# Kernel tuning notes

Hardware: AMD Instinct MI355X
Metric: run time of the kernel (lower is better)

Reference implementation:

```python
import jax, jax.numpy as jnp
import numpy as np

NUM_HEADS = 8
H_NUM, W_NUM = 1, 2   # idx=0 stripe windows
SCALE = float((256 // NUM_HEADS) ** -0.5)  # qk_scale


def _partition(x, h_sp, w_sp):
    # x: (T,B,C,H,W) -> (T, B*nWin, heads, N, C//heads) with N = h_sp*w_sp
    T, B, C, H, W = x.shape
    x = x.reshape(T, B, C, H // h_sp, h_sp, W // w_sp, w_sp)
    x = x.transpose(0, 1, 3, 5, 4, 6, 2)  # T,B,nH,nW,h_sp,w_sp,C
    x = x.reshape(T, -1, h_sp * w_sp, NUM_HEADS, C // NUM_HEADS)
    return x.transpose(0, 1, 3, 2, 4)


def setup_inputs() -> dict:
    key = jax.random.key(0)
    k1, k2, k3 = jax.random.split(key, 3)
    shape = (4, 2, 256, 56, 56)
    return {
        "q": jax.random.normal(k1, shape, jnp.float32),
        "k": jax.random.normal(k2, shape, jnp.float32),
        "v": jax.random.normal(k3, shape, jnp.float32),
        "v_lamda": 1,
    }


def reference(q, k, v, v_lamda):
    T, B, C, H0, W0 = q.shape
    h_pad = (-H0) % H_NUM
    w_pad = (-W0) % W_NUM
    pad = ((0, 0), (0, 0), (0, 0), (0, h_pad), (0, w_pad))
    q = jnp.pad(q, pad)
    k = jnp.pad(k, pad)
    v = jnp.pad(v, pad)
    H, W = H0 + h_pad, W0 + w_pad
    h_sp, w_sp = H // H_NUM, W // W_NUM

    qw = _partition(q, h_sp, w_sp)  # (T, BnW, h, N, d)
    kw = _partition(k, h_sp, w_sp)
    vw = _partition(v, h_sp, w_sp)  # head dim = C*v_lamda//heads

    attn = jnp.einsum('twhnd,twhmd->twhnm', qw, kw)          # (QK^T), no softmax
    out = jnp.einsum('twhnm,twhmd->twhnd', attn, vw) * (SCALE * 2)

    # merge windows back: (T,BnW,h,N,d) -> (T,B,Cv,H,W)
    Cv = C * v_lamda
    out = out.transpose(0, 1, 3, 2, 4).reshape(T, -1, h_sp * w_sp, Cv)
    out = out.reshape(T, B, H_NUM, W_NUM, h_sp, w_sp, Cv)
    out = out.transpose(0, 1, 2, 4, 3, 5, 6).reshape(T, B, H, W, Cv)
    out = out.transpose(0, 1, 4, 2, 3)
    return out[:, :, :, :H0, :W0]
```

## Files before the change

### kernel.cpp

```cpp
#include <hip/hip_runtime.h>


#define TDIM 4
#define BDIM 2
#define CDIM 256
#define HDIM 56
#define WDIM 56
#define DHEAD 32
#define WSP 28
#define NPOS 1568
#define HW 3136
#define NPROB 128
#define SPLIT 4
#define NP_SPLIT 392
#define CHUNK 56
#define NCHUNK 7
#define LDSTRIDE 57
#define SCALE2 0.35355339059327373f

__global__ __launch_bounds__(256) void kv_kernel(const float* __restrict__ K,
                                                 const float* __restrict__ V,
                                                 float* __restrict__ M) {
    __shared__ float kT[32 * LDSTRIDE];
    __shared__ float vT[32 * LDSTRIDE];
    __shared__ float red[4 * 1024];

    const int blk  = blockIdx.x;
    const int p    = blk >> 2;
    const int s    = blk & 3;
    const int head = p & 7;
    const int win  = (p >> 3) & 1;
    const int b    = (p >> 4) & 1;
    const int t    = p >> 5;

    const long base = ((long)(t * BDIM + b) * CDIM + head * DHEAD) * HW;
    const float* __restrict__ Kb = K + base;
    const float* __restrict__ Vb = V + base;

    const int tid = threadIdx.x;
    const int l   = tid & 63;
    const int w   = tid >> 6;
    const int dd0 = (l >> 3) * 4;
    const int de0 = (l & 7) * 4;

    float acc[4][4] = {};

    const int n_base = s * NP_SPLIT;
    for (int c = 0; c < NCHUNK; ++c) {
        const int n0 = n_base + c * CHUNK;
        #pragma unroll
        for (int jj = 0; jj < 7; ++jj) {
            const int idx = tid + 256 * jj;
            const int ch  = idx / 56;
            const int pp  = idx - ch * 56;
            const int n   = n0 + pp;
            const int y   = n / 28;
            const int x   = win * 28 + (n - y * 28);
            const int ga  = ch * HW + y * WDIM + x;
            kT[ch * LDSTRIDE + pp] = Kb[ga];
            vT[ch * LDSTRIDE + pp] = Vb[ga];
        }
        __syncthreads();
        const int pbeg = w * 14;
        for (int pp = pbeg; pp < pbeg + 14; ++pp) {
            float kv[4], vv[4];
            #pragma unroll
            for (int i = 0; i < 4; ++i) kv[i] = kT[(dd0 + i) * LDSTRIDE + pp];
            #pragma unroll
            for (int j = 0; j < 4; ++j) vv[j] = vT[(de0 + j) * LDSTRIDE + pp];
            #pragma unroll
            for (int i = 0; i < 4; ++i)
                #pragma unroll
                for (int j = 0; j < 4; ++j)
                    acc[i][j] += kv[i] * vv[j];
        }
        __syncthreads();
    }

    #pragma unroll
    for (int i = 0; i < 4; ++i)
        #pragma unroll
        for (int j = 0; j < 4; ++j)
            red[w * 1024 + (dd0 + i) * 32 + (de0 + j)] = acc[i][j];
    __syncthreads();
    #pragma unroll
    for (int jj = 0; jj < 4; ++jj) {
        const int m = tid * 4 + jj;
        const float sum = red[m] + red[1024 + m] + red[2048 + m] + red[3072 + m];
        atomicAdd(&M[p * 1024 + m], sum);
    }
}

__global__ __launch_bounds__(256) void qm_kernel(const float* __restrict__ Q,
                                                 const float* __restrict__ M,
                                                 float* __restrict__ Out) {
    const int blk = blockIdx.x;
    const int p   = blk / 7;
    const int c   = blk - p * 7;
    const int n   = c * 256 + threadIdx.x;

    const int head = p & 7;
    const int win  = (p >> 3) & 1;
    const int b    = (p >> 4) & 1;
    const int t    = p >> 5;
    const float* __restrict__ Mp = M + p * 1024;

    if (n >= NPOS) return;

    const int y = n / 28;
    const int x = win * 28 + (n - y * 28);
    const long base = ((long)(t * BDIM + b) * CDIM + head * DHEAD) * HW
                    + y * WDIM + x;
    const float* __restrict__ Qb = Q + base;
    float* __restrict__ Ob = Out + base;

    float acc[32] = {};
    #pragma unroll 4
    for (int dd = 0; dd < 32; ++dd) {
        const float qv = Qb[dd * HW];
        #pragma unroll
        for (int de = 0; de < 32; ++de)
            acc[de] += qv * Mp[dd * 32 + de];
    }
    #pragma unroll
    for (int de = 0; de < 32; ++de)
        Ob[de * HW] = acc[de] * SCALE2;
}

extern "C" void kernel_launch(void* const* d_in, const int* in_sizes, int n_in,
                              void* d_out, int out_size, void* d_ws, size_t ws_size,
                              hipStream_t stream) {
    const float* q = (const float*)d_in[0];
    const float* k = (const float*)d_in[1];
    const float* v = (const float*)d_in[2];
    float* out = (float*)d_out;
    float* M   = (float*)d_ws;

    hipMemsetAsync(M, 0, NPROB * 1024 * sizeof(float), stream);
    kv_kernel<<<NPROB * SPLIT, 256, 0, stream>>>(k, v, M);
    qm_kernel<<<NPROB * 7, 256, 0, stream>>>(q, M, out);
}
```

Baseline: 132.9 us.

## Split KV reduction wider, write partials, reduce in QM kernel without atomics

The K^T V kernel now splits each problem into 14 blocks instead of 4. Each block loads its whole 112-position slice once into a transposed LDS layout so it can use float4 reads, and writes a per-block partial matrix instead of using atomicAdd. This removes the memset launch and the atomic contention. The QM kernel sums the 14 partials into shared memory, applies the scale there, and reads M with float4 loads from LDS. The trade-off is a larger workspace and repeated partial reduction in every QM block (7 blocks per problem), and 32 of the 256 threads in each QM block now idle.

```diff
diff --git a/kernel.cpp b/kernel.cpp
--- a/kernel.cpp
+++ b/kernel.cpp
@@ -1,130 +1,150 @@
 #include <hip/hip_runtime.h>
 
 
-#define TDIM 4
-#define BDIM 2
-#define CDIM 256
-#define HDIM 56
+#define HW 3136
 #define WDIM 56
-#define DHEAD 32
-#define WSP 28
 #define NPOS 1568
-#define HW 3136
 #define NPROB 128
-#define SPLIT 4
-#define NP_SPLIT 392
-#define CHUNK 56
-#define NCHUNK 7
-#define LDSTRIDE 57
+#define SPLIT 14
+#define PSPLIT 112
+#define LROW 36
 #define SCALE2 0.35355339059327373f
 
 __global__ __launch_bounds__(256) void kv_kernel(const float* __restrict__ K,
                                                  const float* __restrict__ V,
-                                                 float* __restrict__ M) {
-    __shared__ float kT[32 * LDSTRIDE];
-    __shared__ float vT[32 * LDSTRIDE];
-    __shared__ float red[4 * 1024];
+                                                 float* __restrict__ Mpart) {
+    __shared__ float lds[2 * PSPLIT * LROW];
+    float* kT = lds;
+    float* vT = lds + PSPLIT * LROW;
 
-    const int blk  = blockIdx.x;
-    const int p    = blk >> 2;
-    const int s    = blk & 3;
+    const int blk = blockIdx.x;
+    const int p   = blk / SPLIT;
+    const int s   = blk - p * SPLIT;
     const int head = p & 7;
     const int win  = (p >> 3) & 1;
     const int b    = (p >> 4) & 1;
     const int t    = p >> 5;
 
-    const long base = ((long)(t * BDIM + b) * CDIM + head * DHEAD) * HW;
+    const size_t base = (size_t)((t * 2 + b) * 256 + head * 32) * HW;
     const float* __restrict__ Kb = K + base;
     const float* __restrict__ Vb = V + base;
 
     const int tid = threadIdx.x;
+
+    #pragma unroll
+    for (int j = 0; j < 7; ++j) {
+        const int item = tid + 256 * j;
+        const int isv  = item >= 896 ? 1 : 0;
+        const int r    = item - isv * 896;
+        const int chg  = r / 112;
+        const int pp   = r - chg * 112;
+        const int n  = s * PSPLIT + pp;
+        const int y  = n / 28;
+        const int x  = n - y * 28;
+        const float* src = (isv ? Vb : Kb)
+                         + (size_t)chg * 4 * HW + y * WDIM + win * 28 + x;
+        float4 val;
+        val.x = src[0];
+        val.y = src[HW];
+        val.z = src[2 * HW];
+        val.w = src[3 * HW];
+        float* dst = isv ? vT : kT;
+        *(float4*)&dst[pp * LROW + chg * 4] = val;
+    }
+    __syncthreads();
+
     const int l   = tid & 63;
     const int w   = tid >> 6;
     const int dd0 = (l >> 3) * 4;
     const int de0 = (l & 7) * 4;
 
-    float acc[4][4] = {};
-
-    const int n_base = s * NP_SPLIT;
-    for (int c = 0; c < NCHUNK; ++c) {
-        const int n0 = n_base + c * CHUNK;
-        #pragma unroll
-        for (int jj = 0; jj < 7; ++jj) {
-            const int idx = tid + 256 * jj;
-            const int ch  = idx / 56;
-            const int pp  = idx - ch * 56;
-            const int n   = n0 + pp;
-            const int y   = n / 28;
-            const int x   = win * 28 + (n - y * 28);
-            const int ga  = ch * HW + y * WDIM + x;
-            kT[ch * LDSTRIDE + pp] = Kb[ga];
-            vT[ch * LDSTRIDE + pp] = Vb[ga];
-        }
-        __syncthreads();
-        const int pbeg = w * 14;
-        for (int pp = pbeg; pp < pbeg + 14; ++pp) {
-            float kv[4], vv[4];
-            #pragma unroll
-            for (int i = 0; i < 4; ++i) kv[i] = kT[(dd0 + i) * LDSTRIDE + pp];
-            #pragma unroll
-            for (int j = 0; j < 4; ++j) vv[j] = vT[(de0 + j) * LDSTRIDE + pp];
-            #pragma unroll
-            for (int i = 0; i < 4; ++i)
-                #pragma unroll
-                for (int j = 0; j < 4; ++j)
-                    acc[i][j] += kv[i] * vv[j];
-        }
-        __syncthreads();
+    float acc[4][4] = {{0.f}};
+    const int p0 = w * 28;
+    #pragma unroll 4
+    for (int pp = p0; pp < p0 + 28; ++pp) {
+        const float4 ka = *(const float4*)&kT[pp * LROW + dd0];
+        const float4 va = *(const float4*)&vT[pp * LROW + de0];
+        acc[0][0] += ka.x * va.x; acc[0][1] += ka.x * va.y;
+        acc[0][2] += ka.x * va.z; acc[0][3] += ka.x * va.w;
+        acc[1][0] += ka.y * va.x; acc[1][1] += ka.y * va.y;
+        acc[1][2] += ka.y * va.z; acc[1][3] += ka.y * va.w;
+        acc[2][0] += ka.z * va.x; acc[2][1] += ka.z * va.y;
+        acc[2][2] += ka.z * va.z; acc[2][3] += ka.z * va.w;
+        acc[3][0] += ka.w * va.x; acc[3][1] += ka.w * va.y;
+        acc[3][2] += ka.w * va.z; acc[3][3] += ka.w * va.w;
     }
+    __syncthreads();
 
     #pragma unroll
     for (int i = 0; i < 4; ++i)
         #pragma unroll
-        for (int j = 0; j < 4; ++j)
-            red[w * 1024 + (dd0 + i) * 32 + (de0 + j)] = acc[i][j];
+        for (int jj = 0; jj < 4; ++jj)
+            lds[w * 1024 + (dd0 + i) * 32 + (de0 + jj)] = acc[i][jj];
     __syncthreads();
-    #pragma unroll
-    for (int jj = 0; jj < 4; ++jj) {
-        const int m = tid * 4 + jj;
-        const float sum = red[m] + red[1024 + m] + red[2048 + m] + red[3072 + m];
-        atomicAdd(&M[p * 1024 + m], sum);
-    }
+
+    const float4 r0 = *(const float4*)&lds[tid * 4];
+    const float4 r1 = *(const float4*)&lds[1024 + tid * 4];
+    const float4 r2 = *(const float4*)&lds[2048 + tid * 4];
+    const float4 r3 = *(const float4*)&lds[3072 + tid * 4];
+    float4 o;
+    o.x = r0.x + r1.x + r2.x + r3.x;
+    o.y = r0.y + r1.y + r2.y + r3.y;
+    o.z = r0.z + r1.z + r2.z + r3.z;
+    o.w = r0.w + r1.w + r2.w + r3.w;
+    *(float4*)&Mpart[(size_t)blk * 1024 + tid * 4] = o;
 }
 
 __global__ __launch_bounds__(256) void qm_kernel(const float* __restrict__ Q,
-                                                 const float* __restrict__ M,
+                                                 const float* __restrict__ Mpart,
                                                  float* __restrict__ Out) {
+    __shared__ float M[1024];
     const int blk = blockIdx.x;
     const int p   = blk / 7;
     const int c   = blk - p * 7;
-    const int n   = c * 256 + threadIdx.x;
+    const int tid = threadIdx.x;
+
+    const float* mp = Mpart + (size_t)p * SPLIT * 1024 + tid * 4;
+    float4 sum = {0.f, 0.f, 0.f, 0.f};
+    #pragma unroll
+    for (int s = 0; s < SPLIT; ++s) {
+        const float4 v = *(const float4*)&mp[s * 1024];
+        sum.x += v.x; sum.y += v.y; sum.z += v.z; sum.w += v.w;
+    }
+    sum.x *= SCALE2; sum.y *= SCALE2; sum.z *= SCALE2; sum.w *= SCALE2;
+    *(float4*)&M[tid * 4] = sum;
+    __syncthreads();
 
     const int head = p & 7;
     const int win  = (p >> 3) & 1;
     const int b    = (p >> 4) & 1;
     const int t    = p >> 5;
-    const float* __restrict__ Mp = M + p * 1024;
 
-    if (n >= NPOS) return;
+    if (tid < 224) {
+        const int n = c * 224 + tid;
+        const int y = n / 28;
+        const int x = n - y * 28;
+        const size_t base = (size_t)((t * 2 + b) * 256 + head * 32) * HW
+                          + y * WDIM + win * 28 + x;
+        const float* __restrict__ Qb = Q + base;
+        float* __restrict__ Ob = Out + base;
 
-    const int y = n / 28;
-    const int x = win * 28 + (n - y * 28);
-    const long base = ((long)(t * BDIM + b) * CDIM + head * DHEAD) * HW
-                    + y * WDIM + x;
-    const float* __restrict__ Qb = Q + base;
-    float* __restrict__ Ob = Out + base;
-
-    float acc[32] = {};
-    #pragma unroll 4
-    for (int dd = 0; dd < 32; ++dd) {
-        const float qv = Qb[dd * HW];
+        float acc[32] = {0.f};
+        #pragma unroll 8
+        for (int dd = 0; dd < 32; ++dd) {
+            const float qv = Qb[(size_t)dd * HW];
+            #pragma unroll
+            for (int g = 0; g < 8; ++g) {
+                const float4 m = *(const float4*)&M[dd * 32 + g * 4];
+                acc[g * 4 + 0] += qv * m.x;
+                acc[g * 4 + 1] += qv * m.y;
+                acc[g * 4 + 2] += qv * m.z;
+                acc[g * 4 + 3] += qv * m.w;
+            }
+        }
         #pragma unroll
         for (int de = 0; de < 32; ++de)
-            acc[de] += qv * Mp[dd * 32 + de];
+            Ob[(size_t)de * HW] = acc[de];
     }
-    #pragma unroll
-    for (int de = 0; de < 32; ++de)
-        Ob[de * HW] = acc[de] * SCALE2;
 }
 
 extern "C" void kernel_launch(void* const* d_in, const int* in_sizes, int n_in,
@@ -133,10 +153,9 @@
     const float* q = (const float*)d_in[0];
     const float* k = (const float*)d_in[1];
     const float* v = (const float*)d_in[2];
-    float* out = (float*)d_out;
-    float* M   = (float*)d_ws;
+    float* out   = (float*)d_out;
+    float* Mpart = (float*)d_ws;
 
-    hipMemsetAsync(M, 0, NPROB * 1024 * sizeof(float), stream);
-    kv_kernel<<<NPROB * SPLIT, 256, 0, stream>>>(k, v, M);
-    qm_kernel<<<NPROB * 7, 256, 0, stream>>>(q, M, out);
+    kv_kernel<<<NPROB * SPLIT, 256, 0, stream>>>(k, v, Mpart);
+    qm_kernel<<<NPROB * 7, 256, 0, stream>>>(q, Mpart, out);
 }
```

Result: faster. 129.4 us (-2.6%).
